# Performance work log

Hardware: AMD Instinct MI355X
Metric: run time of the kernel (lower is better)

Reference implementation:

```python
import jax, jax.numpy as jnp
import numpy as np

B = 64            # number of graphs
N_PER = 2048      # nodes per graph (equal-size graphs -> static shapes)
N = B * N_PER     # total nodes
E = 4194304       # total edges (avg degree 32)
C = 256           # in_channels
RATIO = 0.5
K = int(np.ceil(RATIO * N_PER))  # nodes kept per graph


def setup_inputs() -> dict:
    key = jax.random.key(0)
    k1, k2, k3 = jax.random.split(key, 3)
    x = jax.random.normal(k1, (N, C), dtype=jnp.float32)
    edge_index = jax.random.randint(k2, (2, E), 0, N, dtype=jnp.int32)
    query_vec = jax.random.normal(k3, (C,), dtype=jnp.float32)
    batch = (jnp.arange(N, dtype=jnp.int32) // N_PER).astype(jnp.int32)
    return {"x": x, "edge_index": edge_index, "query_vec": query_vec, "batch": batch}


def reference(x, edge_index, query_vec, batch):
    # score via einsum, min_score=None => tanh nonlinearity
    score = jnp.tanh(jnp.einsum("nc,c->n", x, query_vec))           # [N]

    # per-graph top-k (equal-size graphs => reshape + lax.top_k)
    score2 = score.reshape(B, N_PER)                                  # [B, n]
    _, idx = jax.lax.top_k(score2, K)                                 # [B, K]
    perm = (idx + (jnp.arange(B, dtype=idx.dtype) * N_PER)[:, None]).reshape(-1)  # [B*K]

    score_perm = score[perm]                                          # [B*K]
    x_out = x[perm] * score_perm[:, None]                             # multiplier == 1
    batch_out = batch[perm]

    # filter_adj: relabel kept nodes 0..B*K-1, drop edges touching removed nodes.
    # Static-shape variant: dropped edges are marked with -1 instead of compacted.
    node_idx = jnp.full((N,), -1, dtype=jnp.int32).at[perm].set(
        jnp.arange(B * K, dtype=jnp.int32))
    new_ei = node_idx[edge_index]                                     # [2, E]
    edge_mask = (new_ei[0] >= 0) & (new_ei[1] >= 0)                   # [E]
    new_ei = jnp.where(edge_mask[None, :], new_ei, -1)

    return x_out, new_ei, batch_out, perm, score_perm
```

## Files before the change

kernel.cpp:

```cpp
#include <hip/hip_runtime.h>

#define NNODES   131072
#define NPER     2048
#define NGRAPH   64
#define KKEEP    1024
#define NCH      256
#define NEDGE    4194304

#define OFF_EI    16777216
#define OFF_BATCH 25165824
#define OFF_PERM  25231360
#define OFF_SCP   25296896

__device__ __forceinline__ float xla_tanhf(float x) {
  const float kClamp = 7.90531110763549805f;
  float xc = fminf(fmaxf(x, -kClamp), kClamp);
  float x2 = __fmul_rn(xc, xc);
  float p;
  p = __fadd_rn(__fmul_rn(x2, -2.76076847742355e-16f), 2.00018790482477e-13f);
  p = __fadd_rn(__fmul_rn(x2, p), -8.60467152213735e-11f);
  p = __fadd_rn(__fmul_rn(x2, p), 5.12229709037114e-08f);
  p = __fadd_rn(__fmul_rn(x2, p), 1.48572235717979e-05f);
  p = __fadd_rn(__fmul_rn(x2, p), 6.37261928875436e-04f);
  p = __fadd_rn(__fmul_rn(x2, p), 4.89352455891786e-03f);
  float num = __fmul_rn(xc, p);
  float q;
  q = __fadd_rn(__fmul_rn(x2, 1.19825839466702e-06f), 1.18534705686654e-04f);
  q = __fadd_rn(__fmul_rn(x2, q), 2.26843463243900e-03f);
  q = __fadd_rn(__fmul_rn(x2, q), 4.89352518554385e-03f);
  float r = __fdiv_rn(num, q);
  return (fabsf(x) < 0.0004f) ? x : r;
}

__global__ __launch_bounds__(256) void k_score(const float* __restrict__ x,
                                               const float* __restrict__ qv,
                                               float* __restrict__ score) {
  __shared__ float xs[32 * 264];
  __shared__ float qs[256];
  const int t = threadIdx.x;
  const int bid = blockIdx.x;
  qs[t] = qv[t];
  const float* xblk = x + (size_t)bid * 32 * 256;
#pragma unroll
  for (int it = 0; it < 8; ++it) {
    int flat = it * 1024 + t * 4;
    int row = flat >> 8, col = flat & 255;
    float4 v = *reinterpret_cast<const float4*>(xblk + flat);
    *reinterpret_cast<float4*>(&xs[row * 264 + col]) = v;
  }
  __syncthreads();
  const int node = t >> 3;
  const int j = t & 7;
  const float* xr = &xs[node * 264];
  float a = 0.0f;
#pragma unroll
  for (int i = 0; i < 32; ++i) {
    int c = 8 * i + j;
    a = __fadd_rn(__fmul_rn(xr[c], qs[c]), a);
  }
  float s = __fadd_rn(a, __shfl_xor(a, 4, 64));
  s = __fadd_rn(s, __shfl_xor(s, 2, 64));
  s = __fadd_rn(s, __shfl_xor(s, 1, 64));
  if (j == 0) score[bid * 32 + node] = xla_tanhf(s);
}

__global__ __launch_bounds__(1024) void k_topk(const float* __restrict__ score,
                                               unsigned short* __restrict__ tbl,
                                               unsigned int* __restrict__ maskG,
                                               float* __restrict__ out) {
  __shared__ unsigned long long keys[NPER];
  __shared__ unsigned int mask[NPER / 32];
  const int b = blockIdx.x;
  const int t = threadIdx.x;
  if (t < NPER / 32) mask[t] = 0u;
#pragma unroll
  for (int e = t; e < NPER; e += 1024) {
    float s = score[b * NPER + e];
    unsigned u = __float_as_uint(s);
    unsigned ks = (u & 0x80000000u) ? ~u : (u | 0x80000000u);
    keys[e] = ((unsigned long long)(~ks) << 32) | (unsigned long long)(unsigned)e;
  }
  __syncthreads();
  for (int k = 2; k <= NPER; k <<= 1) {
    for (int j = k >> 1; j > 0; j >>= 1) {
      const bool cross = (j > 64);
      if (cross) __syncthreads();
      int i = ((t & ~(j - 1)) << 1) | (t & (j - 1));
      int pr = i | j;
      bool up = ((i & k) == 0);
      unsigned long long a = keys[i], c = keys[pr];
      if ((c < a) == up) { keys[i] = c; keys[pr] = a; }
      if (cross) __syncthreads();
      else asm volatile("s_waitcnt lgkmcnt(0)" ::: "memory");
    }
  }
  __syncthreads();
  int loc = -1;
  if (t < KKEEP) {
    unsigned long long key = keys[t];
    loc = (int)(unsigned)(key & 0xFFFFFFFFull);
    int g = b * NPER + loc;
    int o = b * KKEEP + t;
    out[OFF_PERM + o]  = (float)g;
    out[OFF_BATCH + o] = (float)b;
    out[OFF_SCP + o]   = score[g];
    tbl[g] = (unsigned short)t;
    atomicOr(&mask[loc >> 5], 1u << (loc & 31));
  }
  __syncthreads();
  if (t < NPER / 32) maskG[b * (NPER / 32) + t] = mask[t];
}

__global__ __launch_bounds__(256) void k_fused(const float* __restrict__ x,
                                               const int* __restrict__ ei,
                                               const unsigned short* __restrict__ tbl,
                                               const unsigned int* __restrict__ maskG,
                                               float* __restrict__ out) {
  const int b = blockIdx.x;
  if (b % 5 == 0) {
    const int tid = (b / 5) * 256 + threadIdx.x;
    int4 s4 = reinterpret_cast<const int4*>(ei)[tid];
    int4 d4 = reinterpret_cast<const int4*>(ei + NEDGE)[tid];
    float4 o0, o1;
#define REL(sv, dv, os, od)                                                    \
    { unsigned mw0 = maskG[(unsigned)sv >> 5], mw1 = maskG[(unsigned)dv >> 5]; \
      bool valid = ((mw0 >> (sv & 31)) & (mw1 >> (dv & 31)) & 1u) != 0u;       \
      os = -1.0f; od = -1.0f;                                                  \
      if (valid) {                                                             \
        unsigned short la = tbl[sv], lb = tbl[dv];                             \
        os = (float)(((sv >> 11) << 10) + la);                                 \
        od = (float)(((dv >> 11) << 10) + lb); } }
    REL(s4.x, d4.x, o0.x, o1.x)
    REL(s4.y, d4.y, o0.y, o1.y)
    REL(s4.z, d4.z, o0.z, o1.z)
    REL(s4.w, d4.w, o0.w, o1.w)
#undef REL
    float* oei = out + OFF_EI;
    reinterpret_cast<float4*>(oei)[tid] = o0;
    reinterpret_cast<float4*>(oei + NEDGE)[tid] = o1;
  } else {
    const int gb = b - (b / 5) - 1;
    const int r = gb * 4 + (threadIdx.x >> 6);
    const int lane = threadIdx.x & 63;
    const int p = (int)out[OFF_PERM + r];
    const float s = out[OFF_SCP + r];
    float4 v = reinterpret_cast<const float4*>(x)[(size_t)p * 64 + lane];
    float4 o;
    o.x = __fmul_rn(v.x, s); o.y = __fmul_rn(v.y, s);
    o.z = __fmul_rn(v.z, s); o.w = __fmul_rn(v.w, s);
    reinterpret_cast<float4*>(out)[(size_t)r * 64 + lane] = o;
  }
}

extern "C" void kernel_launch(void* const* d_in, const int* in_sizes, int n_in,
                              void* d_out, int out_size, void* d_ws, size_t ws_size,
                              hipStream_t stream) {
  const float* x  = (const float*)d_in[0];
  const int*   ei = (const int*)d_in[1];
  const float* qv = (const float*)d_in[2];
  float* out = (float*)d_out;

  float*          score = (float*)d_ws;
  unsigned short* tbl   = (unsigned short*)((char*)d_ws + 524288);
  unsigned int*   maskG = (unsigned int*)((char*)d_ws + 786432);

  k_score<<<4096, 256, 0, stream>>>(x, qv, score);
  k_topk<<<NGRAPH, 1024, 0, stream>>>(score, tbl, maskG, out);
  k_fused<<<20480, 256, 0, stream>>>(x, ei, tbl, maskG, out);
}
```

Baseline: 78.32 us.

## Register-resident bitonic sort with wave shuffles in top-k kernel

Rewrites the per-graph bitonic sort so each thread holds two keys in registers. Compare-exchange steps with partner distance up to 32 threads use wave shuffles, and only larger strides go through padded LDS with block barriers. The score output is decoded from the sort key instead of being re-read from global memory. This cuts LDS traffic and barrier count in a kernel that only launches 64 blocks, at the cost of more shuffle instructions and a key-decoding step that must reproduce the original float bits exactly.

```diff
diff --git a/kernel.cpp b/kernel.cpp
--- a/kernel.cpp
+++ b/kernel.cpp
@@ -68,44 +68,85 @@
                                                unsigned short* __restrict__ tbl,
                                                unsigned int* __restrict__ maskG,
                                                float* __restrict__ out) {
-  __shared__ unsigned long long keys[NPER];
+  __shared__ unsigned long long lds[NPER + (NPER >> 4)];
   __shared__ unsigned int mask[NPER / 32];
   const int b = blockIdx.x;
   const int t = threadIdx.x;
   if (t < NPER / 32) mask[t] = 0u;
-#pragma unroll
-  for (int e = t; e < NPER; e += 1024) {
-    float s = score[b * NPER + e];
-    unsigned u = __float_as_uint(s);
-    unsigned ks = (u & 0x80000000u) ? ~u : (u | 0x80000000u);
-    keys[e] = ((unsigned long long)(~ks) << 32) | (unsigned long long)(unsigned)e;
-  }
+
+  unsigned long long key0, key1;
+  {
+    float2 s2 = reinterpret_cast<const float2*>(score + b * NPER)[t];
+    unsigned u0 = __float_as_uint(s2.x), u1 = __float_as_uint(s2.y);
+    unsigned ks0 = (u0 & 0x80000000u) ? ~u0 : (u0 | 0x80000000u);
+    unsigned ks1 = (u1 & 0x80000000u) ? ~u1 : (u1 | 0x80000000u);
+    key0 = ((unsigned long long)(~ks0) << 32) | (unsigned)(2 * t);
+    key1 = ((unsigned long long)(~ks1) << 32) | (unsigned)(2 * t + 1);
+  }
+
+  {
+    bool up = ((t & 1) == 0);
+    if ((key1 < key0) == up) { unsigned long long tm = key0; key0 = key1; key1 = tm; }
+  }
+
+  for (int k = 4; k <= NPER; k <<= 1) {
+    const int kk = k >> 1;
+    for (int j = kk; j >= 2; j >>= 1) {
+      const int m = j >> 1;
+      const bool keepMin = (((t & m) == 0) == ((t & kk) == 0));
+      if (m <= 32) {
+        unsigned lo0 = (unsigned)key0, hi0 = (unsigned)(key0 >> 32);
+        unsigned lo1 = (unsigned)key1, hi1 = (unsigned)(key1 >> 32);
+        unsigned plo0 = __shfl_xor(lo0, m, 64), phi0 = __shfl_xor(hi0, m, 64);
+        unsigned plo1 = __shfl_xor(lo1, m, 64), phi1 = __shfl_xor(hi1, m, 64);
+        unsigned long long o0 = ((unsigned long long)phi0 << 32) | plo0;
+        unsigned long long o1 = ((unsigned long long)phi1 << 32) | plo1;
+        key0 = ((o0 < key0) == keepMin) ? o0 : key0;
+        key1 = ((o1 < key1) == keepMin) ? o1 : key1;
+      } else {
+        const int e0 = 2 * t, e1 = 2 * t + 1;
+        __syncthreads();
+        lds[e0 + (e0 >> 4)] = key0;
+        lds[e1 + (e1 >> 4)] = key1;
+        __syncthreads();
+        const int p0 = e0 ^ (2 * m);
+        unsigned long long o0 = lds[p0 + (p0 >> 4)];
+        unsigned long long o1 = lds[p0 + 1 + ((p0 + 1) >> 4)];
+        key0 = ((o0 < key0) == keepMin) ? o0 : key0;
+        key1 = ((o1 < key1) == keepMin) ? o1 : key1;
+      }
+    }
+    {
+      bool up = ((t & kk) == 0);
+      if ((key1 < key0) == up) { unsigned long long tm = key0; key0 = key1; key1 = tm; }
+    }
+  }
+
   __syncthreads();
-  for (int k = 2; k <= NPER; k <<= 1) {
-    for (int j = k >> 1; j > 0; j >>= 1) {
-      const bool cross = (j > 64);
-      if (cross) __syncthreads();
-      int i = ((t & ~(j - 1)) << 1) | (t & (j - 1));
-      int pr = i | j;
-      bool up = ((i & k) == 0);
-      unsigned long long a = keys[i], c = keys[pr];
-      if ((c < a) == up) { keys[i] = c; keys[pr] = a; }
-      if (cross) __syncthreads();
-      else asm volatile("s_waitcnt lgkmcnt(0)" ::: "memory");
-    }
-  }
-  __syncthreads();
-  int loc = -1;
-  if (t < KKEEP) {
-    unsigned long long key = keys[t];
-    loc = (int)(unsigned)(key & 0xFFFFFFFFull);
-    int g = b * NPER + loc;
-    int o = b * KKEEP + t;
-    out[OFF_PERM + o]  = (float)g;
-    out[OFF_BATCH + o] = (float)b;
-    out[OFF_SCP + o]   = score[g];
-    tbl[g] = (unsigned short)t;
-    atomicOr(&mask[loc >> 5], 1u << (loc & 31));
+  if (t < 512) {
+    int pos0 = 2 * t;
+    int loc0 = (int)(unsigned)(key0 & 0xFFFFFFFFull);
+    int g0 = b * NPER + loc0;
+    int o0 = b * KKEEP + pos0;
+    out[OFF_PERM + o0]  = (float)g0;
+    out[OFF_BATCH + o0] = (float)b;
+    unsigned rk0 = ~(unsigned)(key0 >> 32);
+    unsigned ru0 = (rk0 & 0x80000000u) ? (rk0 & 0x7FFFFFFFu) : ~rk0;
+    out[OFF_SCP + o0] = __uint_as_float(ru0);
+    tbl[g0] = (unsigned short)pos0;
+    atomicOr(&mask[loc0 >> 5], 1u << (loc0 & 31));
+
+    int pos1 = 2 * t + 1;
+    int loc1 = (int)(unsigned)(key1 & 0xFFFFFFFFull);
+    int g1 = b * NPER + loc1;
+    int o1 = b * KKEEP + pos1;
+    out[OFF_PERM + o1]  = (float)g1;
+    out[OFF_BATCH + o1] = (float)b;
+    unsigned rk1 = ~(unsigned)(key1 >> 32);
+    unsigned ru1 = (rk1 & 0x80000000u) ? (rk1 & 0x7FFFFFFFu) : ~rk1;
+    out[OFF_SCP + o1] = __uint_as_float(ru1);
+    tbl[g1] = (unsigned short)pos1;
+    atomicOr(&mask[loc1 >> 5], 1u << (loc1 & 31));
   }
   __syncthreads();
   if (t < NPER / 32) maskG[b * (NPER / 32) + t] = mask[t];
```

After: 76.86 us, median of 2. Within noise of the previous version (-1.9%).
